# Kernel optimization log

Hardware: AMD Instinct MI355X
Metric: run time of the kernel (lower is better)

The kernel has to match this reference:

```python
import jax, jax.numpy as jnp
import numpy as np

B, T, C = 8, 2048, 1024
HEAD = 64

def setup_inputs() -> dict:
    key = jax.random.key(0)
    k1, k2 = jax.random.split(key)
    x = jax.random.normal(k1, (B, T, C), dtype=jnp.float32)
    W_qkv = jax.random.normal(k2, (C, 3 * HEAD), dtype=jnp.float32) * (C ** -0.5)
    return {"x": x, "W_qkv": W_qkv}

def reference(x, W_qkv):
    # qkv projection (bias-free Linear): [B,T,3*HEAD]
    qkv = x @ W_qkv
    q, k, v = jnp.split(qkv, 3, axis=-1)  # each [B,T,HEAD]
    # scaled dot-product scores [B,T,T]
    dots = jnp.einsum('btd,bsd->bts', q, k) * (HEAD ** -0.5)
    # causal mask (tril == keep)
    Tq = x.shape[1]
    causal = jnp.tril(jnp.ones((Tq, Tq), dtype=bool))
    dots = jnp.where(causal, dots, -jnp.inf)
    attn = jax.nn.softmax(dots, axis=-1)
    # dropout p=0.0 (eval) -> identity
    out = jnp.einsum('bts,bsd->btd', attn, v)  # [B,T,HEAD]
    return out
```

## Files before the change

kernel.cpp:

```cpp
#include <hip/hip_runtime.h>
#include <stdint.h>

#define NB 8
#define NT 2048
#define NC 1024
#define HD 64

typedef __attribute__((ext_vector_type(8)))  short s16x8;
typedef __attribute__((ext_vector_type(4)))  float f32x4;
typedef __attribute__((ext_vector_type(16))) float f32x16;

__device__ inline ushort f2b(float f) {
    union { float f; uint32_t u; } c; c.f = f;
    uint32_t u = c.u;
    uint32_t r = (u + 0x7fffu + ((u >> 16) & 1u)) >> 16;
    return (ushort)r;
}

__device__ inline uint32_t cvt_pk_bf16(float lo, float hi) {
    uint32_t r;
    asm("v_cvt_pk_bf16_f32 %0, %1, %2" : "=v"(r) : "v"(lo), "v"(hi));
    return r;
}

__device__ inline void gload_lds16(const void* gsrc, void* lds) {
    __builtin_amdgcn_global_load_lds(
        (const __attribute__((address_space(1))) void*)gsrc,
        (__attribute__((address_space(3))) void*)lds, 16, 0, 0);
}

__global__ __launch_bounds__(256) void wprep(const float* __restrict__ W,
                                             ushort* __restrict__ wt) {
    int tid = blockIdx.x * 256 + threadIdx.x;
    int n = tid >> 10;
    int k = tid & 1023;
    float v = W[k * 192 + n];
    if (n < 64) v *= 0.125f * 1.4426950408889634f;
    wt[n * 1024 + k] = f2b(v);
}

__global__ __launch_bounds__(256, 4) void qkv_gemm(const float* __restrict__ x,
                                                   const ushort* __restrict__ wt,
                                                   ushort* __restrict__ qs,
                                                   ushort* __restrict__ kk,
                                                   ushort* __restrict__ vt) {
    __shared__ __align__(16) char Al[2][8192];
    __shared__ __align__(16) char Wl[2][12288];

    const int tid = threadIdx.x;
    const int wv  = tid >> 6;
    const int ls  = tid & 63;
    const int r16 = ls & 15;
    const int hi4 = ls >> 4;
    const int bid = blockIdx.x;
    const int rowtile = bid & 511;
    const int cg  = bid >> 9;
    const int row0 = rowtile * 32;
    const int g   = wv >> 1;
    const int c   = wv & 1;

    const float* xsrc[2];
#pragma unroll
    for (int j = 0; j < 2; ++j) {
        int r = (wv * 2 + j) * 4 + (ls >> 4);
        int slot = (ls & 15) ^ (r & 7);
        xsrc[j] = x + (size_t)(row0 + r) * NC + slot * 4;
    }
    const ushort* wsrc[3];
#pragma unroll
    for (int j = 0; j < 3; ++j) {
        int n = (wv * 3 + j) * 8 + (ls >> 3);
        int slot = (ls & 7) ^ (n & 7);
        wsrc[j] = wt + (size_t)(cg * 96 + n) * 1024 + slot * 8;
    }

    const int key = r16 & 7;
    const int arow = g * 16 + r16;
    int aoff[2];
#pragma unroll
    for (int kq = 0; kq < 2; ++kq)
        aoff[kq] = arow * 256 + (((kq * 8 + hi4 * 2) ^ key) << 4);
    int bnrow[3];
#pragma unroll
    for (int nf = 0; nf < 3; ++nf)
        bnrow[nf] = (c * 48 + nf * 16 + r16) * 128;
    int bkey[2];
#pragma unroll
    for (int kq = 0; kq < 2; ++kq)
        bkey[kq] = (((kq * 4 + hi4) ^ key) << 4);

    f32x4 acc[3];
#pragma unroll
    for (int j = 0; j < 3; ++j)
#pragma unroll
        for (int e = 0; e < 4; ++e) acc[j][e] = 0.f;

    auto STAGE = [&](int t) {
        int bb = t & 1;
#pragma unroll
        for (int j = 0; j < 2; ++j)
            gload_lds16(xsrc[j] + t * 64, &Al[bb][(wv * 2 + j) * 1024]);
#pragma unroll
        for (int j = 0; j < 3; ++j)
            gload_lds16(wsrc[j] + t * 64, &Wl[bb][(wv * 3 + j) * 1024]);
    };

    auto COMPUTE = [&](int bb) {
#pragma unroll
        for (int kq = 0; kq < 2; ++kq) {
            float4 a0 = *(const float4*)(&Al[bb][0] + aoff[kq]);
            float4 a1 = *(const float4*)(&Al[bb][0] + (aoff[kq] ^ 16));
            union { uint32_t w[4]; s16x8 v; } pk;
            pk.w[0] = cvt_pk_bf16(a0.x, a0.y);
            pk.w[1] = cvt_pk_bf16(a0.z, a0.w);
            pk.w[2] = cvt_pk_bf16(a1.x, a1.y);
            pk.w[3] = cvt_pk_bf16(a1.z, a1.w);
            s16x8 af = pk.v;
            s16x8 bf[3];
#pragma unroll
            for (int nf = 0; nf < 3; ++nf)
                bf[nf] = *(const s16x8*)(&Wl[bb][0] + bnrow[nf] + bkey[kq]);
#pragma unroll
            for (int nf = 0; nf < 3; ++nf)
                acc[nf] = __builtin_amdgcn_mfma_f32_16x16x32_bf16(
                    af, bf[nf], acc[nf], 0, 0, 0);
        }
    };

    STAGE(0);

    for (int t = 0; t < 16; ++t) {
        asm volatile("s_waitcnt vmcnt(0)" ::: "memory");
        __builtin_amdgcn_s_barrier();
        if (t < 15) STAGE(t + 1);
        COMPUTE(t & 1);
    }

    const int b = row0 >> 11;
    const int rbase = row0 + g * 16 + hi4 * 4;
#pragma unroll
    for (int nf = 0; nf < 3; ++nf) {
        int colg = cg * 96 + c * 48 + nf * 16 + r16;
        f32x4 v = acc[nf];
        if (colg < 64) {
#pragma unroll
            for (int j = 0; j < 4; ++j)
                qs[(size_t)(rbase + j) * HD + colg] = f2b(v[j]);
        } else if (colg < 128) {
#pragma unroll
            for (int j = 0; j < 4; ++j)
                kk[(size_t)(rbase + j) * HD + (colg - 64)] = f2b(v[j]);
        } else {
            int d = colg - 128;
            union { ushort4 s; ushort u[4]; } pk;
#pragma unroll
            for (int j = 0; j < 4; ++j) pk.u[j] = f2b(v[j]);
            *(ushort4*)(&vt[((size_t)(b * 64 + d)) * NT + (rbase & (NT - 1))]) = pk.s;
        }
    }
}

__global__ __launch_bounds__(512) void attn(const ushort* __restrict__ qs,
                                            const ushort* __restrict__ kk,
                                            const ushort* __restrict__ vt,
                                            float* __restrict__ out) {
    __shared__ float ob[8][64][33];
    __shared__ float ml[8][2][32];

    const int bid  = blockIdx.x;
    const int b    = bid & 7;
    const int tile = 63 - (bid >> 3);
    const int tid  = threadIdx.x;
    const int wv   = tid >> 6;
    const int l    = tid & 63;
    const int qcol = l & 31;
    const int hi   = l >> 5;
    const int r0   = tile * 32;

    const ushort* qb = qs + ((size_t)(b * NT + r0)) * HD;
    const ushort* kb = kk + (size_t)b * NT * HD;
    const ushort* vb = vt + (size_t)b * HD * NT;

    s16x8 qf[4];
#pragma unroll
    for (int c = 0; c < 4; ++c)
        qf[c] = *(const s16x8*)(qb + (size_t)qcol * HD + c * 16 + hi * 8);

    f32x16 o0, o1;
#pragma unroll
    for (int i = 0; i < 16; ++i) { o0[i] = 0.f; o1[i] = 0.f; }
    float m = -3.0e30f, lsum = 0.f;

    if (wv <= tile) {
        s16x8 kf[4], vf[4];
        {
            const ushort* kr = kb + (size_t)(wv * 32 + qcol) * HD;
#pragma unroll
            for (int c = 0; c < 4; ++c)
                kf[c] = *(const s16x8*)(kr + c * 16 + hi * 8);
#pragma unroll
            for (int dt = 0; dt < 2; ++dt)
#pragma unroll
                for (int kc = 0; kc < 2; ++kc)
                    vf[dt * 2 + kc] = *(const s16x8*)(vb + (size_t)(dt * 32 + qcol) * NT
                                                      + wv * 32 + kc * 16 + hi * 8);
        }

        for (int kt = wv; kt <= tile; kt += 8) {
            f32x16 s;
#pragma unroll
            for (int i = 0; i < 16; ++i) s[i] = 0.f;
#pragma unroll
            for (int c = 0; c < 4; ++c)
                s = __builtin_amdgcn_mfma_f32_32x32x16_bf16(kf[c], qf[c], s, 0, 0, 0);

            s16x8 kfn[4], vfn[4];
            const bool more = (kt + 8 <= tile);
            if (more) {
                const ushort* kr = kb + (size_t)((kt + 8) * 32 + qcol) * HD;
#pragma unroll
                for (int c = 0; c < 4; ++c)
                    kfn[c] = *(const s16x8*)(kr + c * 16 + hi * 8);
#pragma unroll
                for (int dt = 0; dt < 2; ++dt)
#pragma unroll
                    for (int kc = 0; kc < 2; ++kc)
                        vfn[dt * 2 + kc] = *(const s16x8*)(vb + (size_t)(dt * 32 + qcol) * NT
                                                           + (kt + 8) * 32 + kc * 16 + hi * 8);
            }

            const bool diag = (kt == tile);
            float p[16];
#pragma unroll
            for (int r = 0; r < 16; ++r) {
                int klocal = (r & 3) + 8 * (r >> 2) + 4 * hi;
                float sv = s[r];
                if (diag && klocal > qcol) sv = -3.0e30f;
                p[r] = sv;
            }
            float pmax = p[0];
#pragma unroll
            for (int r = 1; r < 16; ++r) pmax = fmaxf(pmax, p[r]);
            pmax = fmaxf(pmax, __shfl_xor(pmax, 32));
            float mnew = fmaxf(m, pmax);
            float corr = exp2f(m - mnew);
            m = mnew;
            float rs = 0.f;
#pragma unroll
            for (int r = 0; r < 16; ++r) { p[r] = exp2f(p[r] - mnew); rs += p[r]; }
            rs += __shfl_xor(rs, 32);
            lsum = lsum * corr + rs;
#pragma unroll
            for (int i = 0; i < 16; ++i) { o0[i] *= corr; o1[i] *= corr; }

#pragma unroll
            for (int kc = 0; kc < 2; ++kc) {
                int pb = kc * 8;
                uint32_t a0 = cvt_pk_bf16(p[pb + 0], p[pb + 1]);
                uint32_t a1 = cvt_pk_bf16(p[pb + 2], p[pb + 3]);
                uint32_t b0 = cvt_pk_bf16(p[pb + 4], p[pb + 5]);
                uint32_t b1 = cvt_pk_bf16(p[pb + 6], p[pb + 7]);
                uint32_t a0x = __shfl_xor(a0, 32);
                uint32_t a1x = __shfl_xor(a1, 32);
                uint32_t b0x = __shfl_xor(b0, 32);
                uint32_t b1x = __shfl_xor(b1, 32);
                union { uint32_t w[4]; s16x8 v; } frag;
                frag.w[0] = hi ? b0x : a0;
                frag.w[1] = hi ? b1x : a1;
                frag.w[2] = hi ? b0  : a0x;
                frag.w[3] = hi ? b1  : a1x;
                o0 = __builtin_amdgcn_mfma_f32_32x32x16_bf16(vf[0 * 2 + kc], frag.v, o0, 0, 0, 0);
                o1 = __builtin_amdgcn_mfma_f32_32x32x16_bf16(vf[1 * 2 + kc], frag.v, o1, 0, 0, 0);
            }

            if (more) {
#pragma unroll
                for (int c = 0; c < 4; ++c) kf[c] = kfn[c];
#pragma unroll
                for (int c = 0; c < 4; ++c) vf[c] = vfn[c];
            }
        }
    }

#pragma unroll
    for (int r = 0; r < 16; ++r) {
        int d = (r & 3) + 8 * (r >> 2) + 4 * hi;
        ob[wv][d][qcol]      = o0[r];
        ob[wv][d + 32][qcol] = o1[r];
    }
    if (hi == 0) {
        ml[wv][0][qcol] = m;
        ml[wv][1][qcol] = lsum;
    }
    __syncthreads();

    const int q  = tid >> 4;
    const int j0 = (tid & 15) * 4;
    float mwv[8];
#pragma unroll
    for (int w = 0; w < 8; ++w) mwv[w] = ml[w][0][q];
    float M = mwv[0];
#pragma unroll
    for (int w = 1; w < 8; ++w) M = fmaxf(M, mwv[w]);
    float sw[8]; float L = 0.f;
#pragma unroll
    for (int w = 0; w < 8; ++w) {
        sw[w] = exp2f(mwv[w] - M);
        L += sw[w] * ml[w][1][q];
    }
    float invL = 1.0f / L;
    float vals[4];
#pragma unroll
    for (int j = 0; j < 4; ++j) {
        int d = j0 + j;
        float acc = 0.f;
#pragma unroll
        for (int w = 0; w < 8; ++w) acc += sw[w] * ob[w][d][q];
        vals[j] = acc * invL;
    }
    float* orow = out + ((size_t)(b * NT + r0 + q)) * HD + j0;
    *(float4*)(orow) = make_float4(vals[0], vals[1], vals[2], vals[3]);
}

extern "C" void kernel_launch(void* const* d_in, const int* in_sizes, int n_in,
                              void* d_out, int out_size, void* d_ws, size_t ws_size,
                              hipStream_t stream) {
    const float* x = (const float*)d_in[0];
    const float* W = (const float*)d_in[1];
    float* out = (float*)d_out;

    ushort* qs = (ushort*)d_ws;
    ushort* kk = qs + (size_t)NB * NT * HD;
    ushort* vt = kk + (size_t)NB * NT * HD;
    ushort* wt = vt + (size_t)NB * NT * HD;

    wprep<<<768, 256, 0, stream>>>(W, wt);
    qkv_gemm<<<1024, 256, 0, stream>>>(x, wt, qs, kk, vt);
    attn<<<512, 512, 0, stream>>>(qs, kk, vt, out);
}
```

Before: 50.85 us.

## Restructure QKV GEMM: full-K x tile in LDS, W streamed from registers

Each block now handles 64 rows and all 192 output columns. The full 64x1024 slice of x is converted to bf16 once into a swizzled 128KB LDS buffer. W fragments are streamed straight from global memory into registers with inline-asm loads, double-buffered under hand-placed vmcnt waits. This removes the x re-reads across the two column groups and the per-k-step barriers. The cost is a grid of only 256 blocks at occupancy 1, so fewer waves hide latency, and the x load phase is not overlapped with compute.

```diff
diff --git a/kernel.cpp b/kernel.cpp
--- a/kernel.cpp
+++ b/kernel.cpp
@@ -39,123 +39,153 @@
     wt[n * 1024 + k] = f2b(v);
 }
 
-__global__ __launch_bounds__(256, 4) void qkv_gemm(const float* __restrict__ x,
+#define WL_(dst, base, OFF) \
+    asm volatile("global_load_dwordx4 %0, %1, off offset:" #OFF \
+                 : "=&v"(dst) : "v"(base))
+#define WL(dst, base, OFF) WL_(dst, base, OFF)
+
+#define WSET(WF, OFF) \
+    WL(WF[0][0], wb00, OFF); WL(WF[0][1], wb01, OFF); \
+    WL(WF[1][0], wb10, OFF); WL(WF[1][1], wb11, OFF); \
+    WL(WF[2][0], wb20, OFF); WL(WF[2][1], wb21, OFF)
+
+__global__ __launch_bounds__(256, 1) void qkv_gemm(const float* __restrict__ x,
                                                    const ushort* __restrict__ wt,
                                                    ushort* __restrict__ qs,
                                                    ushort* __restrict__ kk,
                                                    ushort* __restrict__ vt) {
-    __shared__ __align__(16) char Al[2][8192];
-    __shared__ __align__(16) char Wl[2][12288];
+    __shared__ __align__(16) char Alds[131072];
 
     const int tid = threadIdx.x;
     const int wv  = tid >> 6;
     const int ls  = tid & 63;
     const int r16 = ls & 15;
     const int hi4 = ls >> 4;
-    const int bid = blockIdx.x;
-    const int rowtile = bid & 511;
-    const int cg  = bid >> 9;
-    const int row0 = rowtile * 32;
-    const int g   = wv >> 1;
-    const int c   = wv & 1;
-
-    const float* xsrc[2];
-#pragma unroll
-    for (int j = 0; j < 2; ++j) {
-        int r = (wv * 2 + j) * 4 + (ls >> 4);
-        int slot = (ls & 15) ^ (r & 7);
-        xsrc[j] = x + (size_t)(row0 + r) * NC + slot * 4;
-    }
-    const ushort* wsrc[3];
-#pragma unroll
-    for (int j = 0; j < 3; ++j) {
-        int n = (wv * 3 + j) * 8 + (ls >> 3);
-        int slot = (ls & 7) ^ (n & 7);
-        wsrc[j] = wt + (size_t)(cg * 96 + n) * 1024 + slot * 8;
-    }
-
-    const int key = r16 & 7;
-    const int arow = g * 16 + r16;
-    int aoff[2];
-#pragma unroll
-    for (int kq = 0; kq < 2; ++kq)
-        aoff[kq] = arow * 256 + (((kq * 8 + hi4 * 2) ^ key) << 4);
-    int bnrow[3];
-#pragma unroll
-    for (int nf = 0; nf < 3; ++nf)
-        bnrow[nf] = (c * 48 + nf * 16 + r16) * 128;
-    int bkey[2];
-#pragma unroll
-    for (int kq = 0; kq < 2; ++kq)
-        bkey[kq] = (((kq * 4 + hi4) ^ key) << 4);
-
-    f32x4 acc[3];
-#pragma unroll
-    for (int j = 0; j < 3; ++j)
-#pragma unroll
-        for (int e = 0; e < 4; ++e) acc[j][e] = 0.f;
-
-    auto STAGE = [&](int t) {
-        int bb = t & 1;
-#pragma unroll
-        for (int j = 0; j < 2; ++j)
-            gload_lds16(xsrc[j] + t * 64, &Al[bb][(wv * 2 + j) * 1024]);
-#pragma unroll
-        for (int j = 0; j < 3; ++j)
-            gload_lds16(wsrc[j] + t * 64, &Wl[bb][(wv * 3 + j) * 1024]);
-    };
-
-    auto COMPUTE = [&](int bb) {
-#pragma unroll
-        for (int kq = 0; kq < 2; ++kq) {
-            float4 a0 = *(const float4*)(&Al[bb][0] + aoff[kq]);
-            float4 a1 = *(const float4*)(&Al[bb][0] + (aoff[kq] ^ 16));
-            union { uint32_t w[4]; s16x8 v; } pk;
-            pk.w[0] = cvt_pk_bf16(a0.x, a0.y);
-            pk.w[1] = cvt_pk_bf16(a0.z, a0.w);
-            pk.w[2] = cvt_pk_bf16(a1.x, a1.y);
-            pk.w[3] = cvt_pk_bf16(a1.z, a1.w);
-            s16x8 af = pk.v;
-            s16x8 bf[3];
-#pragma unroll
-            for (int nf = 0; nf < 3; ++nf)
-                bf[nf] = *(const s16x8*)(&Wl[bb][0] + bnrow[nf] + bkey[kq]);
-#pragma unroll
-            for (int nf = 0; nf < 3; ++nf)
-                acc[nf] = __builtin_amdgcn_mfma_f32_16x16x32_bf16(
-                    af, bf[nf], acc[nf], 0, 0, 0);
+    const int row0 = blockIdx.x * 64;
+    const int b    = row0 >> 11;
+    const int rloc = row0 & (NT - 1);
+
+    {
+#pragma unroll
+        for (int i = 0; i < 16; ++i) {
+            int pidx = i * 256 + tid;
+            int row  = pidx >> 6;
+            int p    = pidx & 63;
+            const float* src = x + (size_t)(row0 + row) * NC + p * 16;
+            float4 f0 = *(const float4*)(src);
+            float4 f1 = *(const float4*)(src + 4);
+            float4 f2 = *(const float4*)(src + 8);
+            float4 f3 = *(const float4*)(src + 12);
+            union { uint32_t w[4]; s16x8 v; } g0, g1;
+            g0.w[0] = cvt_pk_bf16(f0.x, f0.y);
+            g0.w[1] = cvt_pk_bf16(f0.z, f0.w);
+            g0.w[2] = cvt_pk_bf16(f1.x, f1.y);
+            g0.w[3] = cvt_pk_bf16(f1.z, f1.w);
+            g1.w[0] = cvt_pk_bf16(f2.x, f2.y);
+            g1.w[1] = cvt_pk_bf16(f2.z, f2.w);
+            g1.w[2] = cvt_pk_bf16(f3.x, f3.y);
+            g1.w[3] = cvt_pk_bf16(f3.z, f3.w);
+            int slot = (2 * p) ^ (2 * (row & 7));
+            *(s16x8*)(&Alds[row * 2048 + slot * 16])      = g0.v;
+            *(s16x8*)(&Alds[row * 2048 + slot * 16 + 16]) = g1.v;
         }
-    };
-
-    STAGE(0);
-
-    for (int t = 0; t < 16; ++t) {
-        asm volatile("s_waitcnt vmcnt(0)" ::: "memory");
-        __builtin_amdgcn_s_barrier();
-        if (t < 15) STAGE(t + 1);
-        COMPUTE(t & 1);
-    }
-
-    const int b = row0 >> 11;
-    const int rbase = row0 + g * 16 + hi4 * 4;
-#pragma unroll
-    for (int nf = 0; nf < 3; ++nf) {
-        int colg = cg * 96 + c * 48 + nf * 16 + r16;
-        f32x4 v = acc[nf];
-        if (colg < 64) {
-#pragma unroll
-            for (int j = 0; j < 4; ++j)
-                qs[(size_t)(rbase + j) * HD + colg] = f2b(v[j]);
-        } else if (colg < 128) {
-#pragma unroll
-            for (int j = 0; j < 4; ++j)
-                kk[(size_t)(rbase + j) * HD + (colg - 64)] = f2b(v[j]);
-        } else {
-            int d = colg - 128;
-            union { ushort4 s; ushort u[4]; } pk;
-#pragma unroll
-            for (int j = 0; j < 4; ++j) pk.u[j] = f2b(v[j]);
-            *(ushort4*)(&vt[((size_t)(b * 64 + d)) * NT + (rbase & (NT - 1))]) = pk.s;
+    }
+
+    const int akey = 2 * (r16 & 7);
+    int abase[4];
+#pragma unroll
+    for (int m = 0; m < 4; ++m) abase[m] = (m * 16 + r16) * 2048;
+
+    const ushort* wb00 = wt + (size_t)(wv * 48 + 0 * 16 + r16) * 1024 + 0 * 32 + hi4 * 8;
+    const ushort* wb01 = wt + (size_t)(wv * 48 + 0 * 16 + r16) * 1024 + 1 * 32 + hi4 * 8;
+    const ushort* wb10 = wt + (size_t)(wv * 48 + 1 * 16 + r16) * 1024 + 0 * 32 + hi4 * 8;
+    const ushort* wb11 = wt + (size_t)(wv * 48 + 1 * 16 + r16) * 1024 + 1 * 32 + hi4 * 8;
+    const ushort* wb20 = wt + (size_t)(wv * 48 + 2 * 16 + r16) * 1024 + 0 * 32 + hi4 * 8;
+    const ushort* wb21 = wt + (size_t)(wv * 48 + 2 * 16 + r16) * 1024 + 1 * 32 + hi4 * 8;
+
+    f32x4 acc[4][3];
+#pragma unroll
+    for (int m = 0; m < 4; ++m)
+#pragma unroll
+        for (int nf = 0; nf < 3; ++nf)
+#pragma unroll
+            for (int e = 0; e < 4; ++e) acc[m][nf][e] = 0.f;
+
+    s16x8 wfA[3][2], wfB[3][2];
+
+#define COMP(T, WF) do {                                                      \
+    _Pragma("unroll")                                                         \
+    for (int kq = 0; kq < 2; ++kq) {                                          \
+        s16x8 af[4];                                                          \
+        _Pragma("unroll")                                                     \
+        for (int m = 0; m < 4; ++m) {                                         \
+            int g = ((T) * 8 + kq * 4 + hi4) ^ akey;                          \
+            af[m] = *(const s16x8*)(&Alds[abase[m] + g * 16]);                \
+        }                                                                     \
+        _Pragma("unroll")                                                     \
+        for (int m = 0; m < 4; ++m)                                           \
+            _Pragma("unroll")                                                 \
+            for (int nf = 0; nf < 3; ++nf)                                    \
+                acc[m][nf] = __builtin_amdgcn_mfma_f32_16x16x32_bf16(         \
+                    af[m], WF[nf][kq], acc[m][nf], 0, 0, 0);                  \
+    }                                                                         \
+} while (0)
+
+#define DSTEP(T, OFFA, OFFB)                                                  \
+    asm volatile("s_waitcnt vmcnt(6)" ::: "memory");                          \
+    __builtin_amdgcn_sched_barrier(0);                                        \
+    COMP(T, wfA);                                                             \
+    WSET(wfA, OFFA);                                                          \
+    asm volatile("s_waitcnt vmcnt(6)" ::: "memory");                          \
+    __builtin_amdgcn_sched_barrier(0);                                        \
+    COMP((T) + 1, wfB);                                                       \
+    WSET(wfB, OFFB);
+
+    __syncthreads();
+
+    WSET(wfA, 0);
+    WSET(wfB, 128);
+
+    DSTEP(0,  256,  384)
+    DSTEP(2,  512,  640)
+    DSTEP(4,  768,  896)
+    DSTEP(6,  1024, 1152)
+    DSTEP(8,  1280, 1408)
+    DSTEP(10, 1536, 1664)
+    DSTEP(12, 1792, 1920)
+    asm volatile("s_waitcnt vmcnt(6)" ::: "memory");
+    __builtin_amdgcn_sched_barrier(0);
+    COMP(14, wfA);
+    asm volatile("s_waitcnt vmcnt(0)" ::: "memory");
+    __builtin_amdgcn_sched_barrier(0);
+    COMP(15, wfB);
+
+#undef DSTEP
+#undef COMP
+
+#pragma unroll
+    for (int m = 0; m < 4; ++m) {
+        const int rbase = row0 + m * 16 + hi4 * 4;
+#pragma unroll
+        for (int nf = 0; nf < 3; ++nf) {
+            int colg = wv * 48 + nf * 16 + r16;
+            f32x4 v = acc[m][nf];
+            if (colg < 64) {
+#pragma unroll
+                for (int j = 0; j < 4; ++j)
+                    qs[(size_t)(rbase + j) * HD + colg] = f2b(v[j]);
+            } else if (colg < 128) {
+#pragma unroll
+                for (int j = 0; j < 4; ++j)
+                    kk[(size_t)(rbase + j) * HD + (colg - 64)] = f2b(v[j]);
+            } else {
+                int d = colg - 128;
+                union { ushort4 s; ushort u[4]; } pk;
+#pragma unroll
+                for (int j = 0; j < 4; ++j) pk.u[j] = f2b(v[j]);
+                *(ushort4*)(&vt[((size_t)(b * 64 + d)) * NT
+                                + ((rloc + m * 16 + hi4 * 4) )]) = pk.s;
+            }
         }
     }
 }
@@ -335,6 +365,6 @@
     ushort* wt = vt + (size_t)NB * NT * HD;
 
     wprep<<<768, 256, 0, stream>>>(W, wt);
-    qkv_gemm<<<1024, 256, 0, stream>>>(x, wt, qs, kk, vt);
+    qkv_gemm<<<256, 256, 0, stream>>>(x, wt, qs, kk, vt);
     attn<<<512, 512, 0, stream>>>(qs, kk, vt, out);
 }
```

After: 56.38 us. +10.9%, slower.
